# Performance work log

Hardware: AMD Instinct MI355X
Metric: run time of the kernel (lower is better)

The kernel has to match this reference:

```python
import jax, jax.numpy as jnp
import numpy as np

N_NODES = 100000
N_EDGES = 1600000
N_FEAT = 64
DIM = 32
N_CLASSES = 10
N_GRAPHS = 64
BN_EPS = 1e-5


def setup_inputs() -> dict:
    key = jax.random.key(0)
    ks = jax.random.split(key, 20)
    x = jax.random.normal(ks[0], (N_NODES, N_FEAT), dtype=jnp.float32)
    edge_index = jax.random.randint(ks[1], (2, N_EDGES), 0, N_NODES, dtype=jnp.int64)
    batch = jnp.sort(jax.random.randint(ks[2], (N_NODES,), 0, N_GRAPHS, dtype=jnp.int64))
    s = 0.1
    # conv1 MLP (in=N_FEAT)
    w1a = jax.random.normal(ks[3], (N_FEAT, DIM), dtype=jnp.float32) * s
    b1a = jnp.zeros((DIM,), jnp.float32)
    w1b = jax.random.normal(ks[4], (DIM, DIM), dtype=jnp.float32) * s
    b1b = jnp.zeros((DIM,), jnp.float32)
    # convs 2-5 MLPs stacked [4, DIM, DIM]
    Wa = jax.random.normal(ks[5], (4, DIM, DIM), dtype=jnp.float32) * s
    Ba = jnp.zeros((4, DIM), jnp.float32)
    Wb = jax.random.normal(ks[6], (4, DIM, DIM), dtype=jnp.float32) * s
    Bb = jnp.zeros((4, DIM), jnp.float32)
    bn_gamma = jnp.ones((5, DIM), jnp.float32)
    bn_beta = jnp.zeros((5, DIM), jnp.float32)
    fc1_w = jax.random.normal(ks[7], (DIM, DIM), dtype=jnp.float32) * s
    fc1_b = jnp.zeros((DIM,), jnp.float32)
    fc2_w = jax.random.normal(ks[8], (DIM, N_CLASSES), dtype=jnp.float32) * s
    fc2_b = jnp.zeros((N_CLASSES,), jnp.float32)
    return dict(x=x, edge_index=edge_index, batch=batch,
                w1a=w1a, b1a=b1a, w1b=w1b, b1b=b1b,
                Wa=Wa, Ba=Ba, Wb=Wb, Bb=Bb,
                bn_gamma=bn_gamma, bn_beta=bn_beta,
                fc1_w=fc1_w, fc1_b=fc1_b, fc2_w=fc2_w, fc2_b=fc2_b)


def _gin_aggr(x, src, dst):
    # sum_{j in N(i)} x_j  + x_i   (eps = 0)
    agg = jax.ops.segment_sum(x[src], dst, num_segments=N_NODES)
    return x + agg


def _mlp(h, wa, ba, wb, bb):
    return jax.nn.relu(h @ wa + ba) @ wb + bb


def _bn(h, gamma, beta):
    mu = jnp.mean(h, axis=0)
    var = jnp.mean((h - mu) ** 2, axis=0)  # biased, torch BN training mode
    return (h - mu) * jax.lax.rsqrt(var + BN_EPS) * gamma + beta


def reference(x, edge_index, batch, w1a, b1a, w1b, b1b, Wa, Ba, Wb, Bb,
              bn_gamma, bn_beta, fc1_w, fc1_b, fc2_w, fc2_b):
    src, dst = edge_index[0], edge_index[1]
    # layer 1 (num_features -> dim)
    h = _mlp(_gin_aggr(x, src, dst), w1a, b1a, w1b, b1b)
    h = _bn(jax.nn.relu(h), bn_gamma[0], bn_beta[0])
    # layers 2-5 (dim -> dim)
    for i in range(4):
        h = _mlp(_gin_aggr(h, src, dst), Wa[i], Ba[i], Wb[i], Bb[i])
        h = _bn(jax.nn.relu(h), bn_gamma[i + 1], bn_beta[i + 1])
    # global add pool over graphs
    g = jax.ops.segment_sum(h, batch, num_segments=N_GRAPHS)  # [G, dim]
    g = jax.nn.relu(g @ fc1_w + fc1_b)
    # dropout: eval mode -> identity
    return g @ fc2_w + fc2_b  # [G, num_classes]
```

## Files before the change

kernel.cpp:

```cpp
#include <hip/hip_runtime.h>

#define NN 100000
#define NE 1600000
#define NF 64
#define DM 32
#define NG 64
#define NC 10
#define BN_EPS 1e-5f

#define BSHIFT 8
#define NBUCK ((NN + 255) >> 8)
#define CHUNK 8192
#define NCH ((NE + CHUNK - 1) / CHUNK)

__global__ __launch_bounds__(256) void binA_k(const int* __restrict__ ei,
                                              int* __restrict__ bcnt) {
    __shared__ int h[NBUCK];
    for (int i = threadIdx.x; i < NBUCK; i += 256) h[i] = 0;
    __syncthreads();
    long long base = (long long)blockIdx.x * CHUNK;
    int n = (int)((NE - base < CHUNK) ? (NE - base) : CHUNK);
    for (int i = threadIdx.x; i < n; i += 256) {
        int d = ei[NE + base + i];
        atomicAdd(&h[d >> BSHIFT], 1);
    }
    __syncthreads();
    for (int i = threadIdx.x; i < NBUCK; i += 256)
        if (h[i]) atomicAdd(&bcnt[i], h[i]);
}

__global__ __launch_bounds__(512) void binB_k(const int* __restrict__ bcnt,
                                              int* __restrict__ bbase,
                                              int* __restrict__ bcur) {
    __shared__ int s[512];
    int t = threadIdx.x;
    int v = (t < NBUCK) ? bcnt[t] : 0;
    s[t] = v;
    __syncthreads();
    int acc = v;
    for (int off = 1; off < 512; off <<= 1) {
        int add = (t >= off) ? s[t - off] : 0;
        __syncthreads();
        acc += add;
        s[t] = acc;
        __syncthreads();
    }
    if (t < NBUCK) { bbase[t] = acc - v; bcur[t] = acc - v; }
    if (t == 0) bbase[NBUCK] = NE;
}

__global__ __launch_bounds__(256) void binC_k(const int* __restrict__ ei,
                                              int* __restrict__ bcur,
                                              unsigned* __restrict__ binned) {
    __shared__ int cnt[NBUCK];
    __shared__ int ofs[NBUCK];
    __shared__ int idx[NBUCK];
    for (int i = threadIdx.x; i < NBUCK; i += 256) { cnt[i] = 0; idx[i] = 0; }
    __syncthreads();
    long long base = (long long)blockIdx.x * CHUNK;
    int n = (int)((NE - base < CHUNK) ? (NE - base) : CHUNK);
    int d[CHUNK / 256];
#pragma unroll
    for (int k = 0; k < CHUNK / 256; k++) {
        int i = threadIdx.x + k * 256;
        int dd = (i < n) ? ei[NE + base + i] : -1;
        d[k] = dd;
        if (dd >= 0) atomicAdd(&cnt[dd >> BSHIFT], 1);
    }
    __syncthreads();
    for (int i = threadIdx.x; i < NBUCK; i += 256)
        if (cnt[i]) ofs[i] = atomicAdd(&bcur[i], cnt[i]);
    __syncthreads();
#pragma unroll
    for (int k = 0; k < CHUNK / 256; k++) {
        int i = threadIdx.x + k * 256;
        if (i < n) {
            unsigned src = (unsigned)ei[base + i];
            int b = d[k] >> BSHIFT;
            int l = atomicAdd(&idx[b], 1);
            binned[ofs[b] + l] = (src << 8) | (unsigned)(d[k] & 255);
        }
    }
}

__global__ __launch_bounds__(256) void binD_k(const unsigned* __restrict__ binned,
                                              const int* __restrict__ bbase,
                                              int* __restrict__ rowptr,
                                              int* __restrict__ csr) {
    __shared__ int cnt[256];
    __shared__ int cur[256];
    __shared__ int s[256];
    int b = blockIdx.x;
    int e0 = bbase[b], e1 = bbase[b + 1];
    int t = threadIdx.x;
    cnt[t] = 0;
    __syncthreads();
    for (int e = e0 + t; e < e1; e += 256) atomicAdd(&cnt[binned[e] & 255u], 1);
    __syncthreads();
    int v = cnt[t];
    s[t] = v;
    __syncthreads();
    int acc = v;
    for (int off = 1; off < 256; off <<= 1) {
        int add = (t >= off) ? s[t - off] : 0;
        __syncthreads();
        acc += add;
        s[t] = acc;
        __syncthreads();
    }
    int base = e0 + acc - v;
    int node = (b << BSHIFT) + t;
    if (node < NN) rowptr[node] = base;
    cur[t] = base;
    if (b == NBUCK - 1 && t == 0) rowptr[NN] = NE;
    __syncthreads();
    for (int e = e0 + t; e < e1; e += 256) {
        unsigned w = binned[e];
        int p = atomicAdd(&cur[w & 255u], 1);
        csr[p] = (int)(w >> 8);
    }
}

__global__ __launch_bounds__(256) void pre1_k(const float* __restrict__ x,
                                              const float* __restrict__ wa,
                                              float* __restrict__ y) {
    __shared__ float sWa[64 * 32];
    int tid = threadIdx.x;
    for (int i = tid; i < 64 * 32; i += 256) sWa[i] = wa[i];
    __syncthreads();
    int node = blockIdx.x * 256 + tid;
    if (node >= NN) return;
    float t[32];
#pragma unroll
    for (int j = 0; j < 32; j++) t[j] = 0.f;
    const float4* xr = reinterpret_cast<const float4*>(x + (long long)node * 64);
    const float4* w4 = reinterpret_cast<const float4*>(sWa);
    for (int k4 = 0; k4 < 16; k4++) {
        float4 xv = xr[k4];
        int kb = k4 * 4;
#pragma unroll
        for (int q = 0; q < 8; q++) {
            float4 w0 = w4[(kb + 0) * 8 + q];
            float4 w1 = w4[(kb + 1) * 8 + q];
            float4 w2 = w4[(kb + 2) * 8 + q];
            float4 w3 = w4[(kb + 3) * 8 + q];
            t[4 * q + 0] += xv.x * w0.x + xv.y * w1.x + xv.z * w2.x + xv.w * w3.x;
            t[4 * q + 1] += xv.x * w0.y + xv.y * w1.y + xv.z * w2.y + xv.w * w3.y;
            t[4 * q + 2] += xv.x * w0.z + xv.y * w1.z + xv.z * w2.z + xv.w * w3.z;
            t[4 * q + 3] += xv.x * w0.w + xv.y * w1.w + xv.z * w2.w + xv.w * w3.w;
        }
    }
    float4* yr = reinterpret_cast<float4*>(y + (long long)node * 32);
#pragma unroll
    for (int q = 0; q < 8; q++) {
        float4 o;
        o.x = t[4 * q]; o.y = t[4 * q + 1]; o.z = t[4 * q + 2]; o.w = t[4 * q + 3];
        yr[q] = o;
    }
}

__global__ __launch_bounds__(256) void gather32_k(const float* __restrict__ y,
                                                  const int* __restrict__ rowptr,
                                                  const int* __restrict__ csr,
                                                  float* __restrict__ agg) {
    int tid = threadIdx.x;
    int node = blockIdx.x * 32 + tid / 8;
    int l = tid % 8;
    if (node >= NN) return;
    int s = rowptr[node], e = rowptr[node + 1];
    const float4* y4 = reinterpret_cast<const float4*>(y);
    float4 a0 = make_float4(0.f, 0.f, 0.f, 0.f);
    float4 a1 = make_float4(0.f, 0.f, 0.f, 0.f);
    int i = s;
    for (; i + 2 <= e; i += 2) {
        int s0 = csr[i], s1 = csr[i + 1];
        float4 v0 = y4[(long long)s0 * 8 + l];
        float4 v1 = y4[(long long)s1 * 8 + l];
        a0.x += v0.x; a0.y += v0.y; a0.z += v0.z; a0.w += v0.w;
        a1.x += v1.x; a1.y += v1.y; a1.z += v1.z; a1.w += v1.w;
    }
    if (i < e) {
        float4 v = y4[(long long)csr[i] * 8 + l];
        a0.x += v.x; a0.y += v.y; a0.z += v.z; a0.w += v.w;
    }
    a0.x += a1.x; a0.y += a1.y; a0.z += a1.z; a0.w += a1.w;
    reinterpret_cast<float4*>(agg)[(long long)node * 8 + l] = a0;
}

__global__ __launch_bounds__(256) void gather_bn_k(const float* __restrict__ h,
                                                   const int* __restrict__ rowptr,
                                                   const int* __restrict__ csr,
                                                   float* __restrict__ agg,
                                                   const float* __restrict__ st,
                                                   const float* __restrict__ gamma,
                                                   const float* __restrict__ beta) {
    int tid = threadIdx.x;
    int node = blockIdx.x * 32 + tid / 8;
    int l = tid % 8;
    if (node >= NN) return;
    const float invn = 1.0f / NN;
    float sc[4], sh[4];
#pragma unroll
    for (int c = 0; c < 4; c++) {
        int f = 4 * l + c;
        float mu = st[f] * invn;
        float var = st[32 + f] * invn - mu * mu;
        float scale = rsqrtf(var + BN_EPS) * gamma[f];
        sc[c] = scale;
        sh[c] = beta[f] - mu * scale;
    }
    int s = rowptr[node], e = rowptr[node + 1];
    const float4* h4 = reinterpret_cast<const float4*>(h);
    float4 a0 = make_float4(0.f, 0.f, 0.f, 0.f);
    float4 a1 = make_float4(0.f, 0.f, 0.f, 0.f);
    int i = s;
    for (; i + 2 <= e; i += 2) {
        int s0 = csr[i], s1 = csr[i + 1];
        float4 v0 = h4[(long long)s0 * 8 + l];
        float4 v1 = h4[(long long)s1 * 8 + l];
        a0.x += v0.x; a0.y += v0.y; a0.z += v0.z; a0.w += v0.w;
        a1.x += v1.x; a1.y += v1.y; a1.z += v1.z; a1.w += v1.w;
    }
    if (i < e) {
        float4 v = h4[(long long)csr[i] * 8 + l];
        a0.x += v.x; a0.y += v.y; a0.z += v.z; a0.w += v.w;
    }
    a0.x += a1.x; a0.y += a1.y; a0.z += a1.z; a0.w += a1.w;
    float deg = (float)(e - s);
    a0.x = a0.x * sc[0] + deg * sh[0];
    a0.y = a0.y * sc[1] + deg * sh[1];
    a0.z = a0.z * sc[2] + deg * sh[2];
    a0.w = a0.w * sc[3] + deg * sh[3];
    reinterpret_cast<float4*>(agg)[(long long)node * 8 + l] = a0;
}

__global__ __launch_bounds__(256) void mlp1b_k(const float* __restrict__ y,
                                               const float* __restrict__ agg,
                                               const float* __restrict__ ba,
                                               const float* __restrict__ wb,
                                               const float* __restrict__ bb,
                                               float* __restrict__ out,
                                               float* __restrict__ stats) {
    __shared__ float sWb[32 * 32];
    __shared__ float sBa[32], sBb[32];
    __shared__ float sSum[4 * 32], sSq[4 * 32];
    int tid = threadIdx.x;
    for (int i = tid; i < 32 * 32; i += 256) sWb[i] = wb[i];
    if (tid < 32) { sBa[tid] = ba[tid]; sBb[tid] = bb[tid]; }
    __syncthreads();

    int node = blockIdx.x * 256 + tid;
    float r[32];
    if (node < NN) {
        const float4* yr = reinterpret_cast<const float4*>(y + (long long)node * 32);
        const float4* ar = reinterpret_cast<const float4*>(agg + (long long)node * 32);
#pragma unroll
        for (int j = 0; j < 32; j++) r[j] = sBb[j];
        const float4* v4 = reinterpret_cast<const float4*>(sWb);
        for (int k4 = 0; k4 < 8; k4++) {
            float4 yv = yr[k4];
            float4 av = ar[k4];
            int kb = k4 * 4;
            float t0 = fmaxf(yv.x + av.x + sBa[kb + 0], 0.f);
            float t1 = fmaxf(yv.y + av.y + sBa[kb + 1], 0.f);
            float t2 = fmaxf(yv.z + av.z + sBa[kb + 2], 0.f);
            float t3 = fmaxf(yv.w + av.w + sBa[kb + 3], 0.f);
#pragma unroll
            for (int q = 0; q < 8; q++) {
                float4 w0 = v4[(kb + 0) * 8 + q];
                float4 w1 = v4[(kb + 1) * 8 + q];
                float4 w2 = v4[(kb + 2) * 8 + q];
                float4 w3 = v4[(kb + 3) * 8 + q];
                r[4 * q + 0] += t0 * w0.x + t1 * w1.x + t2 * w2.x + t3 * w3.x;
                r[4 * q + 1] += t0 * w0.y + t1 * w1.y + t2 * w2.y + t3 * w3.y;
                r[4 * q + 2] += t0 * w0.z + t1 * w1.z + t2 * w2.z + t3 * w3.z;
                r[4 * q + 3] += t0 * w0.w + t1 * w1.w + t2 * w2.w + t3 * w3.w;
            }
        }
#pragma unroll
        for (int j = 0; j < 32; j++) r[j] = fmaxf(r[j], 0.f);
        float4* orow = reinterpret_cast<float4*>(out + (long long)node * 32);
#pragma unroll
        for (int q = 0; q < 8; q++) {
            float4 o;
            o.x = r[4 * q]; o.y = r[4 * q + 1]; o.z = r[4 * q + 2]; o.w = r[4 * q + 3];
            orow[q] = o;
        }
    } else {
#pragma unroll
        for (int j = 0; j < 32; j++) r[j] = 0.f;
    }

    int lane = tid & 63, wid = tid >> 6;
#pragma unroll
    for (int j = 0; j < 32; j++) {
        float v = r[j], v2 = v * v;
#pragma unroll
        for (int off = 32; off >= 1; off >>= 1) {
            v += __shfl_down(v, off, 64);
            v2 += __shfl_down(v2, off, 64);
        }
        if (lane == 0) { sSum[wid * 32 + j] = v; sSq[wid * 32 + j] = v2; }
    }
    __syncthreads();
    if (tid < 32) {
        float a = sSum[tid] + sSum[32 + tid] + sSum[64 + tid] + sSum[96 + tid];
        float b = sSq[tid] + sSq[32 + tid] + sSq[64 + tid] + sSq[96 + tid];
        atomicAdd(&stats[tid], a);
        atomicAdd(&stats[32 + tid], b);
    }
}

__global__ __launch_bounds__(256) void mlp32_bn_k(float* __restrict__ h,
                                                  const float* __restrict__ agg,
                                                  const float* __restrict__ wa,
                                                  const float* __restrict__ ba,
                                                  const float* __restrict__ wb,
                                                  const float* __restrict__ bb,
                                                  const float* __restrict__ st,
                                                  const float* __restrict__ gamma,
                                                  const float* __restrict__ beta,
                                                  float* __restrict__ statsOut) {
    __shared__ float sWa[32 * 32];
    __shared__ float sWb[32 * 32];
    __shared__ float sBa[32], sBb[32];
    __shared__ float sSc[32], sSh[32];
    __shared__ float sSum[4 * 32], sSq[4 * 32];
    int tid = threadIdx.x;
    for (int i = tid; i < 32 * 32; i += 256) { sWa[i] = wa[i]; sWb[i] = wb[i]; }
    if (tid < 32) {
        sBa[tid] = ba[tid]; sBb[tid] = bb[tid];
        const float invn = 1.0f / NN;
        float mu = st[tid] * invn;
        float var = st[32 + tid] * invn - mu * mu;
        float scale = rsqrtf(var + BN_EPS) * gamma[tid];
        sSc[tid] = scale;
        sSh[tid] = beta[tid] - mu * scale;
    }
    __syncthreads();

    int node = blockIdx.x * 256 + tid;
    float r[32];
    if (node < NN) {
        float t[32];
#pragma unroll
        for (int j = 0; j < 32; j++) t[j] = sBa[j];
        const float4* hr = reinterpret_cast<const float4*>(h + (long long)node * 32);
        const float4* ar = reinterpret_cast<const float4*>(agg + (long long)node * 32);
        const float4* w4 = reinterpret_cast<const float4*>(sWa);
        for (int k4 = 0; k4 < 8; k4++) {
            float4 xv = hr[k4];
            float4 av = ar[k4];
            int kb = k4 * 4;
            float a0 = xv.x * sSc[kb + 0] + sSh[kb + 0] + av.x;
            float a1 = xv.y * sSc[kb + 1] + sSh[kb + 1] + av.y;
            float a2 = xv.z * sSc[kb + 2] + sSh[kb + 2] + av.z;
            float a3 = xv.w * sSc[kb + 3] + sSh[kb + 3] + av.w;
#pragma unroll
            for (int q = 0; q < 8; q++) {
                float4 w0 = w4[(kb + 0) * 8 + q];
                float4 w1 = w4[(kb + 1) * 8 + q];
                float4 w2 = w4[(kb + 2) * 8 + q];
                float4 w3 = w4[(kb + 3) * 8 + q];
                t[4 * q + 0] += a0 * w0.x + a1 * w1.x + a2 * w2.x + a3 * w3.x;
                t[4 * q + 1] += a0 * w0.y + a1 * w1.y + a2 * w2.y + a3 * w3.y;
                t[4 * q + 2] += a0 * w0.z + a1 * w1.z + a2 * w2.z + a3 * w3.z;
                t[4 * q + 3] += a0 * w0.w + a1 * w1.w + a2 * w2.w + a3 * w3.w;
            }
        }
#pragma unroll
        for (int j = 0; j < 32; j++) t[j] = fmaxf(t[j], 0.f);
#pragma unroll
        for (int j = 0; j < 32; j++) r[j] = sBb[j];
        const float4* v4 = reinterpret_cast<const float4*>(sWb);
        for (int k = 0; k < 32; k++) {
            float a = t[k];
#pragma unroll
            for (int q = 0; q < 8; q++) {
                float4 w = v4[k * 8 + q];
                r[4 * q + 0] += a * w.x;
                r[4 * q + 1] += a * w.y;
                r[4 * q + 2] += a * w.z;
                r[4 * q + 3] += a * w.w;
            }
        }
#pragma unroll
        for (int j = 0; j < 32; j++) r[j] = fmaxf(r[j], 0.f);
        float4* orow = reinterpret_cast<float4*>(h + (long long)node * 32);
#pragma unroll
        for (int q = 0; q < 8; q++) {
            float4 o;
            o.x = r[4 * q]; o.y = r[4 * q + 1]; o.z = r[4 * q + 2]; o.w = r[4 * q + 3];
            orow[q] = o;
        }
    } else {
#pragma unroll
        for (int j = 0; j < 32; j++) r[j] = 0.f;
    }

    int lane = tid & 63, wid = tid >> 6;
#pragma unroll
    for (int j = 0; j < 32; j++) {
        float v = r[j], v2 = v * v;
#pragma unroll
        for (int off = 32; off >= 1; off >>= 1) {
            v += __shfl_down(v, off, 64);
            v2 += __shfl_down(v2, off, 64);
        }
        if (lane == 0) { sSum[wid * 32 + j] = v; sSq[wid * 32 + j] = v2; }
    }
    __syncthreads();
    if (tid < 32) {
        float a = sSum[tid] + sSum[32 + tid] + sSum[64 + tid] + sSum[96 + tid];
        float b = sSq[tid] + sSq[32 + tid] + sSq[64 + tid] + sSq[96 + tid];
        atomicAdd(&statsOut[tid], a);
        atomicAdd(&statsOut[32 + tid], b);
    }
}

#define POOL_NPB 512
__global__ __launch_bounds__(256) void pool_bn_k(const float* __restrict__ h,
                                                 const int* __restrict__ batch,
                                                 const float* __restrict__ st,
                                                 const float* __restrict__ gamma,
                                                 const float* __restrict__ beta,
                                                 float* __restrict__ pooled) {
    int tid = threadIdx.x;
    int f = tid & 31;
    int p = tid >> 5;
    int n0 = blockIdx.x * POOL_NPB + p * (POOL_NPB / 8);
    int n1 = n0 + POOL_NPB / 8;
    if (n1 > NN) n1 = NN;
    if (n0 >= NN) return;
    const float invn = 1.0f / NN;
    float mu = st[f] * invn;
    float var = st[32 + f] * invn - mu * mu;
    float sc = rsqrtf(var + BN_EPS) * gamma[f];
    float sh = beta[f] - mu * sc;
    float acc = 0.f;
    int cur = batch[n0];
    for (int n = n0; n < n1; n++) {
        int g = batch[n];
        if (g != cur) {
            atomicAdd(&pooled[cur * 32 + f], acc);
            cur = g;
            acc = 0.f;
        }
        acc += h[(long long)n * 32 + f] * sc + sh;
    }
    atomicAdd(&pooled[cur * 32 + f], acc);
}

__global__ __launch_bounds__(64) void final_k(const float* __restrict__ pooled,
                                              const float* __restrict__ w1,
                                              const float* __restrict__ b1,
                                              const float* __restrict__ w2,
                                              const float* __restrict__ b2,
                                              float* __restrict__ out) {
    int g = threadIdx.x;
    if (g >= NG) return;
    float t[32];
#pragma unroll
    for (int j = 0; j < 32; j++) t[j] = b1[j];
    for (int k = 0; k < 32; k++) {
        float a = pooled[g * 32 + k];
#pragma unroll
        for (int j = 0; j < 32; j++) t[j] += a * w1[k * 32 + j];
    }
#pragma unroll
    for (int j = 0; j < 32; j++) t[j] = fmaxf(t[j], 0.f);
    for (int c = 0; c < NC; c++) {
        float o = b2[c];
#pragma unroll
        for (int k = 0; k < 32; k++) o += t[k] * w2[k * NC + c];
        out[g * NC + c] = o;
    }
}

extern "C" void kernel_launch(void* const* d_in, const int* in_sizes, int n_in,
                              void* d_out, int out_size, void* d_ws, size_t ws_size,
                              hipStream_t stream) {
    const float* x = (const float*)d_in[0];
    const int* ei = (const int*)d_in[1];
    const int* batch = (const int*)d_in[2];
    const float* w1a = (const float*)d_in[3];
    const float* b1a = (const float*)d_in[4];
    const float* w1b = (const float*)d_in[5];
    const float* b1b = (const float*)d_in[6];
    const float* Wa = (const float*)d_in[7];
    const float* Ba = (const float*)d_in[8];
    const float* Wb = (const float*)d_in[9];
    const float* Bb = (const float*)d_in[10];
    const float* bn_gamma = (const float*)d_in[11];
    const float* bn_beta = (const float*)d_in[12];
    const float* fc1w = (const float*)d_in[13];
    const float* fc1b = (const float*)d_in[14];
    const float* fc2w = (const float*)d_in[15];
    const float* fc2b = (const float*)d_in[16];
    float* out = (float*)d_out;

    float* ws = (float*)d_ws;
    float* y = ws;
    float* hb = y + (size_t)NN * 32;
    float* agg = hb + (size_t)NN * 32;
    float* stats_all = agg + (size_t)NN * 32;
    float* pooled = stats_all + 5 * 64;
    unsigned* binned = (unsigned*)(pooled + NG * 32);
    int* bcnt = (int*)(binned + NE);
    int* bbase = bcnt + NBUCK;
    int* bcur = bbase + NBUCK + 1;
    int* rowptr = bcur + NBUCK;
    int* csr = rowptr + NN + 1;

    const int nodeBlocks = (NN + 255) / 256;
    const int gBlocks = (NN + 31) / 32;

    hipMemsetAsync(bcnt, 0, NBUCK * sizeof(int), stream);
    binA_k<<<NCH, 256, 0, stream>>>(ei, bcnt);
    binB_k<<<1, 512, 0, stream>>>(bcnt, bbase, bcur);
    binC_k<<<NCH, 256, 0, stream>>>(ei, bcur, binned);
    binD_k<<<NBUCK, 256, 0, stream>>>(binned, bbase, rowptr, csr);

    hipMemsetAsync(stats_all, 0, (5 * 64 + NG * 32) * sizeof(float), stream);

    pre1_k<<<nodeBlocks, 256, 0, stream>>>(x, w1a, y);
    gather32_k<<<gBlocks, 256, 0, stream>>>(y, rowptr, csr, agg);
    mlp1b_k<<<nodeBlocks, 256, 0, stream>>>(y, agg, b1a, w1b, b1b, hb, stats_all);

    for (int i = 0; i < 4; i++) {
        const float* st = stats_all + i * 64;
        const float* g = bn_gamma + i * 32;
        const float* be = bn_beta + i * 32;
        gather_bn_k<<<gBlocks, 256, 0, stream>>>(hb, rowptr, csr, agg, st, g, be);
        mlp32_bn_k<<<nodeBlocks, 256, 0, stream>>>(hb, agg, Wa + i * 1024, Ba + i * 32,
                                                   Wb + i * 1024, Bb + i * 32,
                                                   st, g, be, stats_all + (i + 1) * 64);
    }

    pool_bn_k<<<(NN + POOL_NPB - 1) / POOL_NPB, 256, 0, stream>>>(
        hb, batch, stats_all + 4 * 64, bn_gamma + 4 * 32, bn_beta + 4 * 32, pooled);
    final_k<<<1, 64, 0, stream>>>(pooled, fc1w, fc1b, fc2w, fc2b, out);
}
```

Measured before the change: 525.3 us.

## Gather neighbor features from fp16 shadow copies instead of fp32

```diff
diff --git a/kernel.cpp b/kernel.cpp
--- a/kernel.cpp
+++ b/kernel.cpp
@@ -1,4 +1,5 @@
 #include <hip/hip_runtime.h>
+#include <hip/hip_fp16.h>
 
 #define NN 100000
 #define NE 1600000
@@ -12,6 +13,15 @@
 #define NBUCK ((NN + 255) >> 8)
 #define CHUNK 8192
 #define NCH ((NE + CHUNK - 1) / CHUNK)
+
+__device__ __forceinline__ float2 up2(unsigned u) {
+    __half2 h = __builtin_bit_cast(__half2, u);
+    return __half22float2(h);
+}
+__device__ __forceinline__ unsigned pk2(float a, float b) {
+    __half2 h = __floats2half2_rn(a, b);
+    return __builtin_bit_cast(unsigned, h);
+}
 
 __global__ __launch_bounds__(256) void binA_k(const int* __restrict__ ei,
                                               int* __restrict__ bcnt) {
@@ -123,9 +133,14 @@
 
 __global__ __launch_bounds__(256) void pre1_k(const float* __restrict__ x,
                                               const float* __restrict__ wa,
-                                              float* __restrict__ y) {
+                                              float* __restrict__ y,
+                                              unsigned* __restrict__ yhf,
+                                              float* __restrict__ zbuf) {
     __shared__ float sWa[64 * 32];
     int tid = threadIdx.x;
+    if (blockIdx.x == 0) {
+        for (int i = tid; i < 5 * 64 + NG * 32; i += 256) zbuf[i] = 0.f;
+    }
     for (int i = tid; i < 64 * 32; i += 256) sWa[i] = wa[i];
     __syncthreads();
     int node = blockIdx.x * 256 + tid;
@@ -157,81 +172,92 @@
         o.x = t[4 * q]; o.y = t[4 * q + 1]; o.z = t[4 * q + 2]; o.w = t[4 * q + 3];
         yr[q] = o;
     }
-}
-
-__global__ __launch_bounds__(256) void gather32_k(const float* __restrict__ y,
-                                                  const int* __restrict__ rowptr,
-                                                  const int* __restrict__ csr,
-                                                  float* __restrict__ agg) {
+    uint4* yb = reinterpret_cast<uint4*>(yhf) + (long long)node * 4;
+#pragma unroll
+    for (int g = 0; g < 4; g++) {
+        uint4 p;
+        p.x = pk2(t[8 * g + 0], t[8 * g + 1]);
+        p.y = pk2(t[8 * g + 2], t[8 * g + 3]);
+        p.z = pk2(t[8 * g + 4], t[8 * g + 5]);
+        p.w = pk2(t[8 * g + 6], t[8 * g + 7]);
+        yb[g] = p;
+    }
+}
+
+template <bool BN>
+__global__ __launch_bounds__(256) void gatherH_k(const unsigned* __restrict__ thf,
+                                                 const int* __restrict__ rowptr,
+                                                 const int* __restrict__ csr,
+                                                 float* __restrict__ agg,
+                                                 const float* __restrict__ st,
+                                                 const float* __restrict__ gamma,
+                                                 const float* __restrict__ beta) {
     int tid = threadIdx.x;
-    int node = blockIdx.x * 32 + tid / 8;
-    int l = tid % 8;
+    int node = blockIdx.x * 64 + (tid >> 2);
+    int l = tid & 3;
     if (node >= NN) return;
+    float sc[8], sh[8];
+    if (BN) {
+        const float invn = 1.0f / NN;
+#pragma unroll
+        for (int c = 0; c < 8; c++) {
+            int f = 8 * l + c;
+            float mu = st[f] * invn;
+            float var = st[32 + f] * invn - mu * mu;
+            float scale = rsqrtf(var + BN_EPS) * gamma[f];
+            sc[c] = scale;
+            sh[c] = beta[f] - mu * scale;
+        }
+    }
     int s = rowptr[node], e = rowptr[node + 1];
-    const float4* y4 = reinterpret_cast<const float4*>(y);
-    float4 a0 = make_float4(0.f, 0.f, 0.f, 0.f);
-    float4 a1 = make_float4(0.f, 0.f, 0.f, 0.f);
+    const uint4* t4 = reinterpret_cast<const uint4*>(thf);
+    float a[8];
+#pragma unroll
+    for (int c = 0; c < 8; c++) a[c] = 0.f;
     int i = s;
-    for (; i + 2 <= e; i += 2) {
-        int s0 = csr[i], s1 = csr[i + 1];
-        float4 v0 = y4[(long long)s0 * 8 + l];
-        float4 v1 = y4[(long long)s1 * 8 + l];
-        a0.x += v0.x; a0.y += v0.y; a0.z += v0.z; a0.w += v0.w;
-        a1.x += v1.x; a1.y += v1.y; a1.z += v1.z; a1.w += v1.w;
-    }
-    if (i < e) {
-        float4 v = y4[(long long)csr[i] * 8 + l];
-        a0.x += v.x; a0.y += v.y; a0.z += v.z; a0.w += v.w;
-    }
-    a0.x += a1.x; a0.y += a1.y; a0.z += a1.z; a0.w += a1.w;
-    reinterpret_cast<float4*>(agg)[(long long)node * 8 + l] = a0;
-}
-
-__global__ __launch_bounds__(256) void gather_bn_k(const float* __restrict__ h,
-                                                   const int* __restrict__ rowptr,
-                                                   const int* __restrict__ csr,
-                                                   float* __restrict__ agg,
-                                                   const float* __restrict__ st,
-                                                   const float* __restrict__ gamma,
-                                                   const float* __restrict__ beta) {
-    int tid = threadIdx.x;
-    int node = blockIdx.x * 32 + tid / 8;
-    int l = tid % 8;
-    if (node >= NN) return;
-    const float invn = 1.0f / NN;
-    float sc[4], sh[4];
-#pragma unroll
-    for (int c = 0; c < 4; c++) {
-        int f = 4 * l + c;
-        float mu = st[f] * invn;
-        float var = st[32 + f] * invn - mu * mu;
-        float scale = rsqrtf(var + BN_EPS) * gamma[f];
-        sc[c] = scale;
-        sh[c] = beta[f] - mu * scale;
-    }
-    int s = rowptr[node], e = rowptr[node + 1];
-    const float4* h4 = reinterpret_cast<const float4*>(h);
-    float4 a0 = make_float4(0.f, 0.f, 0.f, 0.f);
-    float4 a1 = make_float4(0.f, 0.f, 0.f, 0.f);
-    int i = s;
-    for (; i + 2 <= e; i += 2) {
-        int s0 = csr[i], s1 = csr[i + 1];
-        float4 v0 = h4[(long long)s0 * 8 + l];
-        float4 v1 = h4[(long long)s1 * 8 + l];
-        a0.x += v0.x; a0.y += v0.y; a0.z += v0.z; a0.w += v0.w;
-        a1.x += v1.x; a1.y += v1.y; a1.z += v1.z; a1.w += v1.w;
-    }
-    if (i < e) {
-        float4 v = h4[(long long)csr[i] * 8 + l];
-        a0.x += v.x; a0.y += v.y; a0.z += v.z; a0.w += v.w;
-    }
-    a0.x += a1.x; a0.y += a1.y; a0.z += a1.z; a0.w += a1.w;
-    float deg = (float)(e - s);
-    a0.x = a0.x * sc[0] + deg * sh[0];
-    a0.y = a0.y * sc[1] + deg * sh[1];
-    a0.z = a0.z * sc[2] + deg * sh[2];
-    a0.w = a0.w * sc[3] + deg * sh[3];
-    reinterpret_cast<float4*>(agg)[(long long)node * 8 + l] = a0;
+    for (; i + 4 <= e; i += 4) {
+        int s0 = csr[i], s1 = csr[i + 1], s2 = csr[i + 2], s3 = csr[i + 3];
+        uint4 w0 = t4[(long long)s0 * 4 + l];
+        uint4 w1 = t4[(long long)s1 * 4 + l];
+        uint4 w2 = t4[(long long)s2 * 4 + l];
+        uint4 w3 = t4[(long long)s3 * 4 + l];
+        float2 p;
+        p = up2(w0.x); a[0] += p.x; a[1] += p.y;
+        p = up2(w0.y); a[2] += p.x; a[3] += p.y;
+        p = up2(w0.z); a[4] += p.x; a[5] += p.y;
+        p = up2(w0.w); a[6] += p.x; a[7] += p.y;
+        p = up2(w1.x); a[0] += p.x; a[1] += p.y;
+        p = up2(w1.y); a[2] += p.x; a[3] += p.y;
+        p = up2(w1.z); a[4] += p.x; a[5] += p.y;
+        p = up2(w1.w); a[6] += p.x; a[7] += p.y;
+        p = up2(w2.x); a[0] += p.x; a[1] += p.y;
+        p = up2(w2.y); a[2] += p.x; a[3] += p.y;
+        p = up2(w2.z); a[4] += p.x; a[5] += p.y;
+        p = up2(w2.w); a[6] += p.x; a[7] += p.y;
+        p = up2(w3.x); a[0] += p.x; a[1] += p.y;
+        p = up2(w3.y); a[2] += p.x; a[3] += p.y;
+        p = up2(w3.z); a[4] += p.x; a[5] += p.y;
+        p = up2(w3.w); a[6] += p.x; a[7] += p.y;
+    }
+    for (; i < e; i++) {
+        uint4 w = t4[(long long)csr[i] * 4 + l];
+        float2 p;
+        p = up2(w.x); a[0] += p.x; a[1] += p.y;
+        p = up2(w.y); a[2] += p.x; a[3] += p.y;
+        p = up2(w.z); a[4] += p.x; a[5] += p.y;
+        p = up2(w.w); a[6] += p.x; a[7] += p.y;
+    }
+    if (BN) {
+        float deg = (float)(e - s);
+#pragma unroll
+        for (int c = 0; c < 8; c++) a[c] = a[c] * sc[c] + deg * sh[c];
+    }
+    float4* ar = reinterpret_cast<float4*>(agg + (long long)node * 32 + l * 8);
+    float4 o0, o1;
+    o0.x = a[0]; o0.y = a[1]; o0.z = a[2]; o0.w = a[3];
+    o1.x = a[4]; o1.y = a[5]; o1.z = a[6]; o1.w = a[7];
+    ar[0] = o0;
+    ar[1] = o1;
 }
 
 __global__ __launch_bounds__(256) void mlp1b_k(const float* __restrict__ y,
@@ -240,6 +266,7 @@
                                                const float* __restrict__ wb,
                                                const float* __restrict__ bb,
                                                float* __restrict__ out,
+                                               unsigned* __restrict__ outhf,
                                                float* __restrict__ stats) {
     __shared__ float sWb[32 * 32];
     __shared__ float sBa[32], sBb[32];
@@ -286,6 +313,16 @@
             o.x = r[4 * q]; o.y = r[4 * q + 1]; o.z = r[4 * q + 2]; o.w = r[4 * q + 3];
             orow[q] = o;
         }
+        uint4* ob = reinterpret_cast<uint4*>(outhf) + (long long)node * 4;
+#pragma unroll
+        for (int g = 0; g < 4; g++) {
+            uint4 p;
+            p.x = pk2(r[8 * g + 0], r[8 * g + 1]);
+            p.y = pk2(r[8 * g + 2], r[8 * g + 3]);
+            p.z = pk2(r[8 * g + 4], r[8 * g + 5]);
+            p.w = pk2(r[8 * g + 6], r[8 * g + 7]);
+            ob[g] = p;
+        }
     } else {
 #pragma unroll
         for (int j = 0; j < 32; j++) r[j] = 0.f;
@@ -312,6 +349,7 @@
 }
 
 __global__ __launch_bounds__(256) void mlp32_bn_k(float* __restrict__ h,
+                                                  unsigned* __restrict__ hhf,
                                                   const float* __restrict__ agg,
                                                   const float* __restrict__ wa,
                                                   const float* __restrict__ ba,
@@ -392,6 +430,16 @@
             float4 o;
             o.x = r[4 * q]; o.y = r[4 * q + 1]; o.z = r[4 * q + 2]; o.w = r[4 * q + 3];
             orow[q] = o;
+        }
+        uint4* ob = reinterpret_cast<uint4*>(hhf) + (long long)node * 4;
+#pragma unroll
+        for (int g = 0; g < 4; g++) {
+            uint4 p;
+            p.x = pk2(r[8 * g + 0], r[8 * g + 1]);
+            p.y = pk2(r[8 * g + 2], r[8 * g + 3]);
+            p.z = pk2(r[8 * g + 4], r[8 * g + 5]);
+            p.w = pk2(r[8 * g + 6], r[8 * g + 7]);
+            ob[g] = p;
         }
     } else {
 #pragma unroll
@@ -505,7 +553,9 @@
     float* agg = hb + (size_t)NN * 32;
     float* stats_all = agg + (size_t)NN * 32;
     float* pooled = stats_all + 5 * 64;
-    unsigned* binned = (unsigned*)(pooled + NG * 32);
+    unsigned* yhf = (unsigned*)(pooled + NG * 32);
+    unsigned* hbhf = yhf + (size_t)NN * 16;
+    unsigned* binned = hbhf + (size_t)NN * 16;
     int* bcnt = (int*)(binned + NE);
     int* bbase = bcnt + NBUCK;
     int* bcur = bbase + NBUCK + 1;
@@ -513,7 +563,7 @@
     int* csr = rowptr + NN + 1;
 
     const int nodeBlocks = (NN + 255) / 256;
-    const int gBlocks = (NN + 31) / 32;
+    const int gBlocks = (NN + 63) / 64;
 
     hipMemsetAsync(bcnt, 0, NBUCK * sizeof(int), stream);
     binA_k<<<NCH, 256, 0, stream>>>(ei, bcnt);
@@ -521,18 +571,17 @@
     binC_k<<<NCH, 256, 0, stream>>>(ei, bcur, binned);
     binD_k<<<NBUCK, 256, 0, stream>>>(binned, bbase, rowptr, csr);
 
-    hipMemsetAsync(stats_all, 0, (5 * 64 + NG * 32) * sizeof(float), stream);
-
-    pre1_k<<<nodeBlocks, 256, 0, stream>>>(x, w1a, y);
-    gather32_k<<<gBlocks, 256, 0, stream>>>(y, rowptr, csr, agg);
-    mlp1b_k<<<nodeBlocks, 256, 0, stream>>>(y, agg, b1a, w1b, b1b, hb, stats_all);
+    pre1_k<<<nodeBlocks, 256, 0, stream>>>(x, w1a, y, yhf, stats_all);
+    gatherH_k<false><<<gBlocks, 256, 0, stream>>>(yhf, rowptr, csr, agg,
+                                                  nullptr, nullptr, nullptr);
+    mlp1b_k<<<nodeBlocks, 256, 0, stream>>>(y, agg, b1a, w1b, b1b, hb, hbhf, stats_all);
 
     for (int i = 0; i < 4; i++) {
         const float* st = stats_all + i * 64;
         const float* g = bn_gamma + i * 32;
         const float* be = bn_beta + i * 32;
-        gather_bn_k<<<gBlocks, 256, 0, stream>>>(hb, rowptr, csr, agg, st, g, be);
-        mlp32_bn_k<<<nodeBlocks, 256, 0, stream>>>(hb, agg, Wa + i * 1024, Ba + i * 32,
+        gatherH_k<true><<<gBlocks, 256, 0, stream>>>(hbhf, rowptr, csr, agg, st, g, be);
+        mlp32_bn_k<<<nodeBlocks, 256, 0, stream>>>(hb, hbhf, agg, Wa + i * 1024, Ba + i * 32,
                                                    Wb + i * 1024, Bb + i * 32,
                                                    st, g, be, stats_all + (i + 1) * 64);
     }
```

Result: faster. 504.5 us (-4.0%).
